# Kernel tuning notes

Hardware: AMD Instinct MI355X
Metric: run time of the kernel (lower is better)

## Reference

```python
import jax, jax.numpy as jnp
import numpy as np

R = 16
LORA_ALPHA = 32
SCALING = LORA_ALPHA / R  # use_rslora=False -> alpha/r = 2.0


def fwht(x):
    """Normalized fast Walsh-Hadamard transform along last axis (power-of-2 dim)."""
    n = x.shape[-1]
    batch = x.shape[:-1]
    h = 1
    while h < n:  # static loop, log2(n) iterations
        x = x.reshape(*batch, n // (2 * h), 2, h)
        a = x[..., 0, :]
        b = x[..., 1, :]
        x = jnp.stack([a + b, a - b], axis=-2).reshape(*batch, n)
        h *= 2
    return x * np.float32(1.0 / np.sqrt(n))


def quant_int8_ste(x):
    """Simulated symmetric per-row int8 quantization with straight-through estimator."""
    s = jnp.max(jnp.abs(x), axis=-1, keepdims=True) * np.float32(1.0 / 127.0)
    s = jnp.maximum(s, np.float32(1e-8))
    q = jnp.clip(jnp.round(x / s), -127.0, 127.0) * s
    return x + jax.lax.stop_gradient(q - x)


def setup_inputs() -> dict:
    key = jax.random.key(0)
    k1, k2, k3, k4 = jax.random.split(key, 4)
    B, S, D_in, D_out = 4, 2048, 4096, 4096
    x = jax.random.normal(k1, (B, S, D_in), dtype=jnp.float32)
    weight = jax.random.normal(k2, (D_out, D_in), dtype=jnp.float32) * np.float32(0.02)
    lora_A = jax.random.normal(k3, (R, D_in), dtype=jnp.float32) * np.float32(0.02)
    lora_B = jax.random.normal(k4, (D_out, R), dtype=jnp.float32) * np.float32(0.02)
    return {"x": x, "weight": weight, "lora_A": lora_A, "lora_B": lora_B}


def reference(x, weight, lora_A, lora_B):
    B, S, D_in = x.shape
    x2 = x.reshape(-1, D_in)  # [B*S, D_in]
    # Hadamard-rotate + quantize both operands (rotation is orthogonal, so
    # (xH)(WH)^T == xW^T up to quantization error) then GEMM.
    xq = quant_int8_ste(fwht(x2))          # [B*S, D_in]
    wq = quant_int8_ste(fwht(weight))      # [D_out, D_in]
    out = xq @ wq.T                        # [B*S, D_out]
    # LoRA side path (dropout p=0): B(A x) * scaling
    lora = (x2 @ lora_A.T) @ lora_B.T * np.float32(SCALING)
    return (out + lora).reshape(B, S, -1)
```

## Files before the change

### kernel.cpp

```cpp
#include <hip/hip_runtime.h>
#include <stdint.h>

typedef int v4i __attribute__((ext_vector_type(4)));

#define GLD_LDS16(gp, lp)                                                              \
  __builtin_amdgcn_global_load_lds((const __attribute__((address_space(1))) void*)(gp), \
                                   (__attribute__((address_space(3))) void*)(lp), 16, 0, 0)

__device__ __forceinline__ v4i lds_read_b128(uint32_t off) {
  v4i r;
  asm volatile("ds_read_b128 %0, %1" : "=v"(r) : "v"(off));
  return r;
}

#define LGKM_FENCE()                                   \
  do {                                                 \
    asm volatile("s_waitcnt lgkmcnt(0)" ::: "memory"); \
    __builtin_amdgcn_sched_barrier(0);                 \
  } while (0)

__device__ __forceinline__ void fwht16(float v[16]) {
#pragma unroll
  for (int h = 1; h < 16; h <<= 1) {
#pragma unroll
    for (int i = 0; i < 16; ++i) {
      if (!(i & h)) {
        float a = v[i], b = v[i | h];
        v[i] = a + b;
        v[i | h] = a - b;
      }
    }
  }
}

__global__ __launch_bounds__(256) void fwht_quant_kernel(const float* __restrict__ X,
                                                         int8_t* __restrict__ Q,
                                                         float* __restrict__ S) {
  const int row = blockIdx.x;
  const int t = threadIdx.x;
  __shared__ float lds[4224];
  __shared__ float wred[4];

  const float* xr = X + (size_t)row * 4096;
  float v[16];
  {
    const float4* p = reinterpret_cast<const float4*>(xr) + t * 4;
    float4 a = p[0], b = p[1], c = p[2], d = p[3];
    v[0] = a.x; v[1] = a.y; v[2] = a.z; v[3] = a.w;
    v[4] = b.x; v[5] = b.y; v[6] = b.z; v[7] = b.w;
    v[8] = c.x; v[9] = c.y; v[10] = c.z; v[11] = c.w;
    v[12] = d.x; v[13] = d.y; v[14] = d.z; v[15] = d.w;
  }
  fwht16(v);
#pragma unroll
  for (int e = 0; e < 16; ++e) {
    int idx = t * 16 + e;
    lds[idx + (idx >> 5)] = v[e];
  }
  __syncthreads();
#pragma unroll
  for (int e = 0; e < 16; ++e) {
    int idx = ((t >> 4) << 8) + (e << 4) + (t & 15);
    v[e] = lds[idx + (idx >> 5)];
  }
  fwht16(v);
#pragma unroll
  for (int e = 0; e < 16; ++e) {
    int idx = ((t >> 4) << 8) + (e << 4) + (t & 15);
    lds[idx + (idx >> 5)] = v[e];
  }
  __syncthreads();
#pragma unroll
  for (int e = 0; e < 16; ++e) {
    int idx = (e << 8) + t;
    v[e] = lds[idx + (idx >> 5)];
  }
  fwht16(v);

  float m = 0.f;
#pragma unroll
  for (int e = 0; e < 16; ++e) {
    v[e] *= 0.015625f;
    m = fmaxf(m, fabsf(v[e]));
  }
#pragma unroll
  for (int off = 32; off > 0; off >>= 1) m = fmaxf(m, __shfl_xor(m, off));
  if ((t & 63) == 0) wred[t >> 6] = m;
  __syncthreads();
  m = fmaxf(fmaxf(wred[0], wred[1]), fmaxf(wred[2], wred[3]));
  const float s = fmaxf(m * (1.0f / 127.0f), 1e-8f);
  if (t == 0) S[row] = s;
  int8_t* qr = Q + (size_t)row * 4096;
#pragma unroll
  for (int e = 0; e < 16; ++e) {
    float q = rintf(v[e] / s);
    q = fminf(fmaxf(q, -127.f), 127.f);
    qr[(e << 8) + t] = (int8_t)(int)q;
  }
}

__global__ __launch_bounds__(256) void lora_t_partial_kernel(const float* __restrict__ X,
                                                             const float* __restrict__ A,
                                                             float* __restrict__ tpart) {
  __shared__ float As[16][512];
  const int t = threadIdx.x;
  const int kc = blockIdx.y;
  const int row = blockIdx.x * 256 + t;
  for (int i = t; i < 2048; i += 256) {
    int r = i >> 7;
    int c4 = i & 127;
    reinterpret_cast<float4*>(&As[r][0])[c4] =
        reinterpret_cast<const float4*>(A + (size_t)r * 4096 + kc * 512)[c4];
  }
  __syncthreads();
  float acc[16];
#pragma unroll
  for (int r = 0; r < 16; ++r) acc[r] = 0.f;
  const float* xr = X + (size_t)row * 4096 + kc * 512;
  for (int k = 0; k < 512; k += 4) {
    float4 xv = *reinterpret_cast<const float4*>(xr + k);
#pragma unroll
    for (int r = 0; r < 16; ++r) {
      float4 av = *reinterpret_cast<const float4*>(&As[r][k]);
      acc[r] += xv.x * av.x + xv.y * av.y + xv.z * av.z + xv.w * av.w;
    }
  }
  float* tp = tpart + ((size_t)kc * 8192 + row) * 16;
#pragma unroll
  for (int r = 0; r < 16; ++r) tp[r] = acc[r];
}

__global__ __launch_bounds__(256) void lora_t_reduce_kernel(const float* __restrict__ tpart,
                                                            float* __restrict__ tmat) {
  int i = blockIdx.x * 256 + threadIdx.x;
  float s = 0.f;
#pragma unroll
  for (int kc = 0; kc < 8; ++kc) s += tpart[(size_t)kc * 131072 + i];
  tmat[i] = s;
}

__global__ __launch_bounds__(512, 2) void gemm_i8_kernel(
    const int8_t* __restrict__ Aq, const int8_t* __restrict__ Bq,
    const float* __restrict__ Sx, const float* __restrict__ Sw,
    const float* __restrict__ Tm, const float* __restrict__ LB,
    float* __restrict__ out) {
  __shared__ __align__(16) char smem[131072];

  const int tid = threadIdx.x;
  const int lane = tid & 63;
  const int w = tid >> 6;
  const int wm = w >> 2;
  const int wn = w & 3;

  int bid = (int)blockIdx.x;
  bid = (bid & 7) * 64 + (bid >> 3);
  const int bm = bid >> 4;
  const int bn = bid & 15;

  const int8_t* Ag = Aq + (size_t)bm * 256 * 4096;
  const int8_t* Bg = Bq + (size_t)bn * 256 * 4096;

  const uint32_t sbase = (uint32_t)(uintptr_t)(void*)smem;

  const int row0 = w * 32 + (lane >> 3);
  const int srcOff = (((lane & 7) ^ (lane >> 3)) << 4);

#define STAGE_OP(gbase, ldsOpBase, tByte)                                        \
  do {                                                                           \
    _Pragma("unroll") for (int j = 0; j < 4; ++j)                                \
        GLD_LDS16((gbase) + (size_t)(row0 + j * 8) * 4096 + (tByte) + srcOff,    \
                  smem + (ldsOpBase) + w * 4096 + j * 1024);                     \
  } while (0)

  int aoff[8], boff[4];
  const int fch = (((lane >> 4) ^ (lane & 7)) << 4);
#pragma unroll
  for (int mi = 0; mi < 8; ++mi) {
    int r = wm * 128 + mi * 16 + (lane & 15);
    aoff[mi] = r * 128 + fch;
  }
#pragma unroll
  for (int ni = 0; ni < 4; ++ni) {
    int r = wn * 64 + ni * 16 + (lane & 15);
    boff[ni] = 32768 + r * 128 + fch;
  }

  v4i acc[8][4];
#pragma unroll
  for (int i = 0; i < 8; ++i)
#pragma unroll
    for (int n = 0; n < 4; ++n) {
      v4i z = {0, 0, 0, 0};
      acc[i][n] = z;
    }

  STAGE_OP(Ag, 0, 0);
  STAGE_OP(Bg, 32768, 0);
  asm volatile("s_waitcnt vmcnt(0)" ::: "memory");
  __builtin_amdgcn_s_barrier();
  __builtin_amdgcn_sched_barrier(0);

#define MFMA16(MH)                                                                        \
  do {                                                                                    \
    __builtin_amdgcn_s_setprio(1);                                                        \
    _Pragma("unroll") for (int i = 0; i < 4; ++i) _Pragma("unroll") for (int n = 0;       \
                                                                        n < 4; ++n)       \
        acc[(MH)*4 + i][n] =                                                              \
        __builtin_amdgcn_mfma_i32_16x16x64_i8(af[i], bf[n], acc[(MH)*4 + i][n], 0, 0, 0); \
    __builtin_amdgcn_s_setprio(0);                                                        \
  } while (0)

#pragma unroll 1
  for (int t = 0; t < 32; ++t) {
    const uint32_t Ab = sbase + (t & 1) * 65536;
    const int nx = ((t & 1) ^ 1) * 65536;
    const bool pf = (t + 1) < 32;
    const int tB = (t + 1) << 7;
    v4i af[4], bf[4];

    if (pf) {
      STAGE_OP(Ag, nx, tB);
      STAGE_OP(Bg, nx + 32768, tB);
    }

#pragma unroll
    for (int n = 0; n < 4; ++n) bf[n] = lds_read_b128(Ab + boff[n]);
#pragma unroll
    for (int i = 0; i < 4; ++i) af[i] = lds_read_b128(Ab + aoff[i]);
    LGKM_FENCE();
    MFMA16(0);
#pragma unroll
    for (int i = 0; i < 4; ++i) af[i] = lds_read_b128(Ab + aoff[4 + i]);
    LGKM_FENCE();
    MFMA16(1);
#pragma unroll
    for (int n = 0; n < 4; ++n) bf[n] = lds_read_b128(Ab + (boff[n] ^ 64));
#pragma unroll
    for (int i = 0; i < 4; ++i) af[i] = lds_read_b128(Ab + (aoff[i] ^ 64));
    LGKM_FENCE();
    MFMA16(0);
#pragma unroll
    for (int i = 0; i < 4; ++i) af[i] = lds_read_b128(Ab + (aoff[4 + i] ^ 64));
    LGKM_FENCE();
    MFMA16(1);

    asm volatile("s_waitcnt vmcnt(0)" ::: "memory");
    __builtin_amdgcn_s_barrier();
    __builtin_amdgcn_sched_barrier(0);
  }

  __syncthreads();
  float* tl = (float*)smem;
  float* bl = (float*)(smem + 17408);
  for (int i = tid; i < 1024; i += 512) {
    int r = i >> 2, q4 = (i & 3) * 4;
    float4 tv = *reinterpret_cast<const float4*>(Tm + (size_t)(bm * 256 + r) * 16 + q4);
    tl[r * 17 + q4 + 0] = tv.x;
    tl[r * 17 + q4 + 1] = tv.y;
    tl[r * 17 + q4 + 2] = tv.z;
    tl[r * 17 + q4 + 3] = tv.w;
    float4 bv = *reinterpret_cast<const float4*>(LB + (size_t)(bn * 256 + r) * 16 + q4);
    bl[r * 17 + q4 + 0] = bv.x;
    bl[r * 17 + q4 + 1] = bv.y;
    bl[r * 17 + q4 + 2] = bv.z;
    bl[r * 17 + q4 + 3] = bv.w;
  }
  __syncthreads();

  float blv[4][16], swv[4];
#pragma unroll
  for (int ni = 0; ni < 4; ++ni) {
    int cl = wn * 64 + ni * 16 + (lane & 15);
    swv[ni] = Sw[bn * 256 + cl];
#pragma unroll
    for (int q = 0; q < 16; ++q) blv[ni][q] = bl[cl * 17 + q];
  }
#pragma unroll
  for (int mi = 0; mi < 8; ++mi) {
#pragma unroll
    for (int rr = 0; rr < 4; ++rr) {
      int rl = wm * 128 + mi * 16 + (lane >> 4) * 4 + rr;
      float sxv = Sx[bm * 256 + rl];
      float tv[16];
#pragma unroll
      for (int q = 0; q < 16; ++q) tv[q] = tl[rl * 17 + q];
      float* orow = out + (size_t)(bm * 256 + rl) * 4096 + bn * 256;
#pragma unroll
      for (int ni = 0; ni < 4; ++ni) {
        float dot = 0.f;
#pragma unroll
        for (int q = 0; q < 16; ++q) dot = fmaf(tv[q], blv[ni][q], dot);
        int cl = wn * 64 + ni * 16 + (lane & 15);
        orow[cl] = sxv * swv[ni] * (float)acc[mi][ni][rr] + 2.0f * dot;
      }
    }
  }
}

extern "C" void kernel_launch(void* const* d_in, const int* in_sizes, int n_in,
                              void* d_out, int out_size, void* d_ws, size_t ws_size,
                              hipStream_t stream) {
  const float* x = (const float*)d_in[0];
  const float* wgt = (const float*)d_in[1];
  const float* lA = (const float*)d_in[2];
  const float* lB = (const float*)d_in[3];
  float* out = (float*)d_out;

  char* ws = (char*)d_ws;
  int8_t* qx = (int8_t*)ws;
  int8_t* qw = (int8_t*)(ws + 33554432);
  float* sx = (float*)(ws + 50331648);
  float* sw = (float*)(ws + 50364416);
  float* tmat = (float*)(ws + 50380800);
  float* tpart = (float*)(ws + 50905088);

  fwht_quant_kernel<<<8192, 256, 0, stream>>>(x, qx, sx);
  fwht_quant_kernel<<<4096, 256, 0, stream>>>(wgt, qw, sw);
  lora_t_partial_kernel<<<dim3(32, 8), 256, 0, stream>>>(x, lA, tpart);
  lora_t_reduce_kernel<<<512, 256, 0, stream>>>(tpart, tmat);
  gemm_i8_kernel<<<512, 512, 0, stream>>>(qx, qw, sx, sw, tmat, lB, out);
}
```

Before: 265.8 us.

## Deepen GEMM LDS pipeline to four stages and compute LoRA from quantized rotated x

The int8 GEMM main loop now stages 64-byte K slices into a four-buffer LDS ring with a new XOR swizzle. Three slices are prefetched ahead, and it waits with partial vmcnt/lgkmcnt counts instead of draining to zero each step. This aims to overlap global loads with MFMA work and cut barrier stalls. Separately, the LoRA down-projection is computed from the already-quantized Hadamard-rotated int8 x and a Hadamard-rotated lora_A, replacing the fp32 x read. That cuts memory traffic but adds int8 quantization error to the LoRA term.

```diff
diff --git a/kernel.cpp b/kernel.cpp
--- a/kernel.cpp
+++ b/kernel.cpp
@@ -12,12 +12,6 @@
   asm volatile("ds_read_b128 %0, %1" : "=v"(r) : "v"(off));
   return r;
 }
-
-#define LGKM_FENCE()                                   \
-  do {                                                 \
-    asm volatile("s_waitcnt lgkmcnt(0)" ::: "memory"); \
-    __builtin_amdgcn_sched_barrier(0);                 \
-  } while (0)
 
 __device__ __forceinline__ void fwht16(float v[16]) {
 #pragma unroll
@@ -31,6 +25,46 @@
       }
     }
   }
+}
+
+__device__ __forceinline__ void fwht_row_load(const float* __restrict__ xr, int t,
+                                              float v[16]) {
+  const float4* p = reinterpret_cast<const float4*>(xr) + t * 4;
+  float4 a = p[0], b = p[1], c = p[2], d = p[3];
+  v[0] = a.x; v[1] = a.y; v[2] = a.z; v[3] = a.w;
+  v[4] = b.x; v[5] = b.y; v[6] = b.z; v[7] = b.w;
+  v[8] = c.x; v[9] = c.y; v[10] = c.z; v[11] = c.w;
+  v[12] = d.x; v[13] = d.y; v[14] = d.z; v[15] = d.w;
+}
+
+__device__ __forceinline__ void fwht4096(float v[16], float* lds, int t) {
+  fwht16(v);
+#pragma unroll
+  for (int e = 0; e < 16; ++e) {
+    int idx = t * 16 + e;
+    lds[idx + (idx >> 5)] = v[e];
+  }
+  __syncthreads();
+#pragma unroll
+  for (int e = 0; e < 16; ++e) {
+    int idx = ((t >> 4) << 8) + (e << 4) + (t & 15);
+    v[e] = lds[idx + (idx >> 5)];
+  }
+  fwht16(v);
+#pragma unroll
+  for (int e = 0; e < 16; ++e) {
+    int idx = ((t >> 4) << 8) + (e << 4) + (t & 15);
+    lds[idx + (idx >> 5)] = v[e];
+  }
+  __syncthreads();
+#pragma unroll
+  for (int e = 0; e < 16; ++e) {
+    int idx = (e << 8) + t;
+    v[e] = lds[idx + (idx >> 5)];
+  }
+  fwht16(v);
+#pragma unroll
+  for (int e = 0; e < 16; ++e) v[e] *= 0.015625f;
 }
 
 __global__ __launch_bounds__(256) void fwht_quant_kernel(const float* __restrict__ X,
@@ -41,48 +75,13 @@
   __shared__ float lds[4224];
   __shared__ float wred[4];
 
-  const float* xr = X + (size_t)row * 4096;
   float v[16];
-  {
-    const float4* p = reinterpret_cast<const float4*>(xr) + t * 4;
-    float4 a = p[0], b = p[1], c = p[2], d = p[3];
-    v[0] = a.x; v[1] = a.y; v[2] = a.z; v[3] = a.w;
-    v[4] = b.x; v[5] = b.y; v[6] = b.z; v[7] = b.w;
-    v[8] = c.x; v[9] = c.y; v[10] = c.z; v[11] = c.w;
-    v[12] = d.x; v[13] = d.y; v[14] = d.z; v[15] = d.w;
-  }
-  fwht16(v);
-#pragma unroll
-  for (int e = 0; e < 16; ++e) {
-    int idx = t * 16 + e;
-    lds[idx + (idx >> 5)] = v[e];
-  }
-  __syncthreads();
-#pragma unroll
-  for (int e = 0; e < 16; ++e) {
-    int idx = ((t >> 4) << 8) + (e << 4) + (t & 15);
-    v[e] = lds[idx + (idx >> 5)];
-  }
-  fwht16(v);
-#pragma unroll
-  for (int e = 0; e < 16; ++e) {
-    int idx = ((t >> 4) << 8) + (e << 4) + (t & 15);
-    lds[idx + (idx >> 5)] = v[e];
-  }
-  __syncthreads();
-#pragma unroll
-  for (int e = 0; e < 16; ++e) {
-    int idx = (e << 8) + t;
-    v[e] = lds[idx + (idx >> 5)];
-  }
-  fwht16(v);
+  fwht_row_load(X + (size_t)row * 4096, t, v);
+  fwht4096(v, lds, t);
 
   float m = 0.f;
 #pragma unroll
-  for (int e = 0; e < 16; ++e) {
-    v[e] *= 0.015625f;
-    m = fmaxf(m, fabsf(v[e]));
-  }
+  for (int e = 0; e < 16; ++e) m = fmaxf(m, fabsf(v[e]));
 #pragma unroll
   for (int off = 32; off > 0; off >>= 1) m = fmaxf(m, __shfl_xor(m, off));
   if ((t & 63) == 0) wred[t >> 6] = m;
@@ -99,35 +98,55 @@
   }
 }
 
-__global__ __launch_bounds__(256) void lora_t_partial_kernel(const float* __restrict__ X,
-                                                             const float* __restrict__ A,
-                                                             float* __restrict__ tpart) {
+__global__ __launch_bounds__(256) void fwht_nq_kernel(const float* __restrict__ X,
+                                                      float* __restrict__ F) {
+  const int row = blockIdx.x;
+  const int t = threadIdx.x;
+  __shared__ float lds[4224];
+  float v[16];
+  fwht_row_load(X + (size_t)row * 4096, t, v);
+  fwht4096(v, lds, t);
+  float* fr = F + (size_t)row * 4096;
+#pragma unroll
+  for (int e = 0; e < 16; ++e) fr[(e << 8) + t] = v[e];
+}
+
+__global__ __launch_bounds__(256) void lora_t_partial_q(const int8_t* __restrict__ Qx,
+                                                        const float* __restrict__ Sx,
+                                                        const float* __restrict__ Ah,
+                                                        float* __restrict__ tpart) {
   __shared__ float As[16][512];
   const int t = threadIdx.x;
   const int kc = blockIdx.y;
   const int row = blockIdx.x * 256 + t;
   for (int i = t; i < 2048; i += 256) {
-    int r = i >> 7;
-    int c4 = i & 127;
+    int r = i >> 7, c4 = i & 127;
     reinterpret_cast<float4*>(&As[r][0])[c4] =
-        reinterpret_cast<const float4*>(A + (size_t)r * 4096 + kc * 512)[c4];
+        reinterpret_cast<const float4*>(Ah + (size_t)r * 4096 + kc * 512)[c4];
   }
   __syncthreads();
   float acc[16];
 #pragma unroll
   for (int r = 0; r < 16; ++r) acc[r] = 0.f;
-  const float* xr = X + (size_t)row * 4096 + kc * 512;
-  for (int k = 0; k < 512; k += 4) {
-    float4 xv = *reinterpret_cast<const float4*>(xr + k);
-#pragma unroll
-    for (int r = 0; r < 16; ++r) {
-      float4 av = *reinterpret_cast<const float4*>(&As[r][k]);
-      acc[r] += xv.x * av.x + xv.y * av.y + xv.z * av.z + xv.w * av.w;
-    }
-  }
+  const int8_t* xr = Qx + (size_t)row * 4096 + kc * 512;
+  for (int k = 0; k < 512; k += 16) {
+    int4 pv = *reinterpret_cast<const int4*>(xr + k);
+    int us[4] = {pv.x, pv.y, pv.z, pv.w};
+#pragma unroll
+    for (int b = 0; b < 4; ++b) {
+#pragma unroll
+      for (int j = 0; j < 4; ++j) {
+        float f = (float)((int)(int8_t)(us[b] >> (8 * j)));
+        int kk = k + b * 4 + j;
+#pragma unroll
+        for (int r = 0; r < 16; ++r) acc[r] = fmaf(f, As[r][kk], acc[r]);
+      }
+    }
+  }
+  const float s = Sx[row];
   float* tp = tpart + ((size_t)kc * 8192 + row) * 16;
 #pragma unroll
-  for (int r = 0; r < 16; ++r) tp[r] = acc[r];
+  for (int r = 0; r < 16; ++r) tp[r] = acc[r] * s;
 }
 
 __global__ __launch_bounds__(256) void lora_t_reduce_kernel(const float* __restrict__ tpart,
@@ -162,27 +181,30 @@
 
   const uint32_t sbase = (uint32_t)(uintptr_t)(void*)smem;
 
-  const int row0 = w * 32 + (lane >> 3);
-  const int srcOff = (((lane & 7) ^ (lane >> 3)) << 4);
-
-#define STAGE_OP(gbase, ldsOpBase, tByte)                                        \
-  do {                                                                           \
-    _Pragma("unroll") for (int j = 0; j < 4; ++j)                                \
-        GLD_LDS16((gbase) + (size_t)(row0 + j * 8) * 4096 + (tByte) + srcOff,    \
-                  smem + (ldsOpBase) + w * 4096 + j * 1024);                     \
+  const size_t gA0 = (size_t)(w * 32 + (lane >> 2)) * 4096 +
+                     (((lane & 3) ^ ((lane >> 3) & 3)) << 4);
+  const size_t gA1 = gA0 + 16 * 4096;
+
+#define STAGE_STEP(s)                                                   \
+  do {                                                                  \
+    char* dst = smem + ((s) & 3) * 32768 + w * 2048;                    \
+    const size_t kb = (size_t)(s) << 6;                                 \
+    GLD_LDS16(Ag + gA0 + kb, dst);                                      \
+    GLD_LDS16(Ag + gA1 + kb, dst + 1024);                               \
+    GLD_LDS16(Bg + gA0 + kb, dst + 16384);                              \
+    GLD_LDS16(Bg + gA1 + kb, dst + 16384 + 1024);                       \
   } while (0)
 
   int aoff[8], boff[4];
-  const int fch = (((lane >> 4) ^ (lane & 7)) << 4);
 #pragma unroll
   for (int mi = 0; mi < 8; ++mi) {
     int r = wm * 128 + mi * 16 + (lane & 15);
-    aoff[mi] = r * 128 + fch;
+    aoff[mi] = r * 64 + ((((lane >> 4)) ^ ((r >> 1) & 3)) << 4);
   }
 #pragma unroll
   for (int ni = 0; ni < 4; ++ni) {
     int r = wn * 64 + ni * 16 + (lane & 15);
-    boff[ni] = 32768 + r * 128 + fch;
+    boff[ni] = 16384 + r * 64 + ((((lane >> 4)) ^ ((r >> 1) & 3)) << 4);
   }
 
   v4i acc[8][4];
@@ -194,9 +216,10 @@
       acc[i][n] = z;
     }
 
-  STAGE_OP(Ag, 0, 0);
-  STAGE_OP(Bg, 32768, 0);
-  asm volatile("s_waitcnt vmcnt(0)" ::: "memory");
+  STAGE_STEP(0);
+  STAGE_STEP(1);
+  STAGE_STEP(2);
+  asm volatile("s_waitcnt vmcnt(8)" ::: "memory");
   __builtin_amdgcn_s_barrier();
   __builtin_amdgcn_sched_barrier(0);
 
@@ -211,42 +234,36 @@
   } while (0)
 
 #pragma unroll 1
-  for (int t = 0; t < 32; ++t) {
-    const uint32_t Ab = sbase + (t & 1) * 65536;
-    const int nx = ((t & 1) ^ 1) * 65536;
-    const bool pf = (t + 1) < 32;
-    const int tB = (t + 1) << 7;
-    v4i af[4], bf[4];
-
-    if (pf) {
-      STAGE_OP(Ag, nx, tB);
-      STAGE_OP(Bg, nx + 32768, tB);
-    }
-
-#pragma unroll
-    for (int n = 0; n < 4; ++n) bf[n] = lds_read_b128(Ab + boff[n]);
-#pragma unroll
-    for (int i = 0; i < 4; ++i) af[i] = lds_read_b128(Ab + aoff[i]);
-    LGKM_FENCE();
+  for (int t = 0; t < 64; ++t) {
+    const uint32_t bufR = sbase + (t & 3) * 32768;
+    if (t <= 60) STAGE_STEP(t + 3);
+
+    v4i af[4], bf[4], af2[4];
+#pragma unroll
+    for (int n = 0; n < 4; ++n) bf[n] = lds_read_b128(bufR + boff[n]);
+#pragma unroll
+    for (int i = 0; i < 4; ++i) af[i] = lds_read_b128(bufR + aoff[i]);
+#pragma unroll
+    for (int i = 0; i < 4; ++i) af2[i] = lds_read_b128(bufR + aoff[4 + i]);
+    asm volatile("s_waitcnt lgkmcnt(4)" ::: "memory");
+    __builtin_amdgcn_sched_barrier(0);
     MFMA16(0);
 #pragma unroll
-    for (int i = 0; i < 4; ++i) af[i] = lds_read_b128(Ab + aoff[4 + i]);
-    LGKM_FENCE();
+    for (int i = 0; i < 4; ++i) af[i] = af2[i];
+    asm volatile("s_waitcnt lgkmcnt(0)" ::: "memory");
+    __builtin_amdgcn_sched_barrier(0);
     MFMA16(1);
-#pragma unroll
-    for (int n = 0; n < 4; ++n) bf[n] = lds_read_b128(Ab + (boff[n] ^ 64));
-#pragma unroll
-    for (int i = 0; i < 4; ++i) af[i] = lds_read_b128(Ab + (aoff[i] ^ 64));
-    LGKM_FENCE();
-    MFMA16(0);
-#pragma unroll
-    for (int i = 0; i < 4; ++i) af[i] = lds_read_b128(Ab + (aoff[4 + i] ^ 64));
-    LGKM_FENCE();
-    MFMA16(1);
-
-    asm volatile("s_waitcnt vmcnt(0)" ::: "memory");
-    __builtin_amdgcn_s_barrier();
-    __builtin_amdgcn_sched_barrier(0);
+
+    if (t <= 60)
+      asm volatile("s_waitcnt vmcnt(8)" ::: "memory");
+    else if (t == 61)
+      asm volatile("s_waitcnt vmcnt(4)" ::: "memory");
+    else if (t == 62)
+      asm volatile("s_waitcnt vmcnt(0)" ::: "memory");
+    if (t < 63) {
+      __builtin_amdgcn_s_barrier();
+      __builtin_amdgcn_sched_barrier(0);
+    }
   }
 
   __syncthreads();
@@ -313,10 +330,12 @@
   float* sw = (float*)(ws + 50364416);
   float* tmat = (float*)(ws + 50380800);
   float* tpart = (float*)(ws + 50905088);
+  float* Ah = (float*)(ws + 55099392);
 
   fwht_quant_kernel<<<8192, 256, 0, stream>>>(x, qx, sx);
   fwht_quant_kernel<<<4096, 256, 0, stream>>>(wgt, qw, sw);
-  lora_t_partial_kernel<<<dim3(32, 8), 256, 0, stream>>>(x, lA, tpart);
+  fwht_nq_kernel<<<16, 256, 0, stream>>>(lA, Ah);
+  lora_t_partial_q<<<dim3(32, 8), 256, 0, stream>>>(qx, sx, Ah, tpart);
   lora_t_reduce_kernel<<<512, 256, 0, stream>>>(tpart, tmat);
   gemm_i8_kernel<<<512, 512, 0, stream>>>(qx, qw, sx, sw, tmat, lB, out);
 }
```

New measurement: 277.2 us. 4.3% more time.
